# Optimization experiments

Measured on AMD Instinct MI355X. Metric: run time of the kernel, lower is better.

The kernel has to match this reference:

```python
import jax, jax.numpy as jnp
import numpy as np

B, N, H = 1, 4096, 2048
NH, HD = 16, H // 16
WINDOW = 4096
EPS = 1e-6
THETA = 10000.0
NEG = -1e30


def rmsnorm(x, w):
    var = jnp.mean(jnp.square(x.astype(jnp.float32)), axis=-1, keepdims=True)
    return (x * jax.lax.rsqrt(var + EPS)).astype(w.dtype) * w


def rotate_half(x):
    x1, x2 = x[..., : x.shape[-1] // 2], x[..., x.shape[-1] // 2 :]
    return jnp.concatenate((-x2, x1), axis=-1)


def setup_inputs() -> dict:
    key = jax.random.key(0)
    k1, k2, k3 = jax.random.split(key, 3)
    x = jax.random.normal(k1, (B, N, H), dtype=jnp.float32)
    w_qkv = jax.random.normal(k2, (H, 3 * H), dtype=jnp.float32) * (1.0 / np.sqrt(H))
    w_out = jax.random.normal(k3, (H, H), dtype=jnp.float32) * (1.0 / np.sqrt(H))
    q_gamma = jnp.ones((HD,), dtype=jnp.float32)
    k_gamma = jnp.ones((HD,), dtype=jnp.float32)
    return {"x": x, "w_qkv": w_qkv, "w_out": w_out, "q_gamma": q_gamma, "k_gamma": k_gamma}


def reference(x, w_qkv, w_out, q_gamma, k_gamma):
    b, n, _ = x.shape
    qkv = jnp.einsum('bnh,hm->bnm', x, w_qkv)  # [b,n,3H]
    q, k, v = jnp.split(qkv, 3, axis=-1)
    # [b, nh, n, hd]
    q = q.reshape(b, n, NH, HD).transpose(0, 2, 1, 3)
    k = k.reshape(b, n, NH, HD).transpose(0, 2, 1, 3)
    v = v.reshape(b, n, NH, HD).transpose(0, 2, 1, 3)
    # qk RMSNorm over head_dim
    q = rmsnorm(q, q_gamma)
    k = rmsnorm(k, k_gamma)
    # RoPE
    inv_freq = 1.0 / (THETA ** (jnp.arange(0, HD, 2, dtype=jnp.float32) / HD))
    t = jnp.arange(n, dtype=jnp.float32)
    freqs = t[:, None] * inv_freq[None, :]          # [n, hd/2]
    emb = jnp.concatenate((freqs, freqs), axis=-1)  # [n, hd]
    cos = jnp.cos(emb)[None, None, :, :]
    sin = jnp.sin(emb)[None, None, :, :]
    q = q * cos + rotate_half(q) * sin
    k = k * cos + rotate_half(k) * sin
    # causal + sliding-window mask (kv not truncated since n == WINDOW)
    kv_len = k.shape[-2]
    q_idx = jnp.arange(n)[:, None] + (kv_len - n)
    k_idx = jnp.arange(kv_len)[None, :]
    mask = (q_idx >= k_idx) & (q_idx - k_idx <= WINDOW)
    scores = jnp.einsum('bhqd,bhkd->bhqk', q, k) / np.sqrt(HD)
    scores = jnp.where(mask[None, None, :, :], scores, NEG)
    attn = jax.nn.softmax(scores, axis=-1)
    out = jnp.einsum('bhqk,bhkd->bhqd', attn, v)
    out = out.transpose(0, 2, 1, 3).reshape(b, n, H)
    return jnp.einsum('bnh,hm->bnm', out, w_out)
```

## Files before the change

### kernel.cpp

```cpp
#include <hip/hip_runtime.h>
#include <stdint.h>

typedef short bf16x8 __attribute__((ext_vector_type(8)));
typedef float f32x4 __attribute__((ext_vector_type(4)));
typedef unsigned short u16;

__device__ __forceinline__ float b2f(u16 u) {
  return __uint_as_float(((unsigned)u) << 16);
}
__device__ __forceinline__ u16 f2b(float f) {
  unsigned u = __float_as_uint(f);
  return (u16)((u + 0x7fffu + ((u >> 16) & 1u)) >> 16);
}

#define NEGINF (-1.0e30f)

__device__ __forceinline__ void gld_lds16(const u16* g, u16* l) {
  __builtin_amdgcn_global_load_lds(
      (const __attribute__((address_space(1))) unsigned int*)(const void*)g,
      (__attribute__((address_space(3))) unsigned int*)(void*)l, 16, 0, 0);
}

__device__ __forceinline__ int swzV(int o) {
  return o ^ ((((o) >> 6) & 7) << 3);
}
__device__ __forceinline__ int swzK(int o) {
  return o ^ ((((o) >> 7) & 7) << 3);
}

__global__ void sniff5(const u16* x, const u16* wq, const u16* wo,
                       const u16* qg, const u16* kg, int* flags) {
  const u16* p;
  int S;
  switch (blockIdx.x) {
    case 0: p = x;  S = 2048; break;
    case 1: p = wq; S = 2048; break;
    case 2: p = wo; S = 2048; break;
    case 3: p = qg; S = 128;  break;
    default: p = kg; S = 128; break;
  }
  __shared__ int cbig, czero;
  if (threadIdx.x == 0) { cbig = 0; czero = 0; }
  __syncthreads();
  int cb = 0, cz = 0;
  for (int i = threadIdx.x; i < S; i += 256) {
    const u16 u = p[i];
    if (((u >> 7) & 0xFF) >= 0xC0) ++cb;
    if (!(i & 1) && u == 0) ++cz;
  }
  atomicAdd(&cbig, cb);
  atomicAdd(&czero, cz);
  __syncthreads();
  if (threadIdx.x == 0)
    flags[blockIdx.x] = (cbig > S / 32 || czero > 3 * S / 8) ? 1 : 0;
}

__global__ __launch_bounds__(256) void conv_in(const void* __restrict__ src,
                                               u16* __restrict__ dst,
                                               const int* __restrict__ flags,
                                               int fidx, int n) {
  const int fp32 = flags[fidx];
  int i = blockIdx.x * 256 + threadIdx.x;
  const int stride = gridDim.x * 256;
  if (fp32) {
    const float* s = (const float*)src;
    for (; i < n; i += stride) dst[i] = f2b(s[i]);
  } else {
    const u16* s = (const u16*)src;
    for (; i < n; i += stride) dst[i] = s[i];
  }
}

__global__ __launch_bounds__(256) void transpose_in(
    const void* __restrict__ src, u16* __restrict__ dst,
    const int* __restrict__ flags, int fidx, int ss, int ds) {
  __shared__ u16 tile[64][65];
  const int fp32 = flags[fidx];
  const int rb = blockIdx.y * 64, cb = blockIdx.x * 64;
  const int cl = threadIdx.x & 63, r0 = threadIdx.x >> 6;
  if (fp32) {
    const float* s = (const float*)src;
#pragma unroll
    for (int i = 0; i < 16; ++i) {
      int r = r0 + i * 4;
      tile[r][cl] = f2b(s[(long long)(rb + r) * ss + cb + cl]);
    }
  } else {
    const u16* s = (const u16*)src;
#pragma unroll
    for (int i = 0; i < 16; ++i) {
      int r = r0 + i * 4;
      tile[r][cl] = s[(long long)(rb + r) * ss + cb + cl];
    }
  }
  __syncthreads();
#pragma unroll
  for (int i = 0; i < 16; ++i) {
    int r2 = r0 + i * 4;
    dst[(long long)(cb + r2) * ds + rb + cl] = tile[cl][r2];
  }
}

__global__ __launch_bounds__(256, 4) void gemm_qkv(
    const u16* __restrict__ A, const u16* __restrict__ Bt,
    const u16* __restrict__ gq, const u16* __restrict__ gk,
    u16* __restrict__ Cq, u16* __restrict__ Ck, u16* __restrict__ Cv, int K) {
  __shared__ __align__(16) u16 smem[2 * 128 * 64];
  u16* As = smem;
  u16* Bs = smem + 128 * 64;
  const int bid = blockIdx.x;
  const int xcd = bid & 7, lid = bid >> 3;
  const int mb = lid / 6, nsub = lid - mb * 6;
  const int nb = xcd * 6 + nsub;
  const int m0 = mb * 128;
  const int n0g = nb * 128;
  const int sel = nb >> 4;
  const int h = nb & 15;
  const int tid = threadIdx.x;
  const int w = tid >> 6, l = tid & 63;
  const int lane15 = l & 15, quad = l >> 4;
  const int wm = (w >> 1) * 64, wn = (w & 1) * 64;
  const int r8 = l >> 3, c8 = l & 7;
  const int sk = (c8 ^ r8) * 8;
  const u16* gA = A + (size_t)(m0 + r8) * K + sk;
  const u16* gB = Bt + (size_t)(n0g + r8) * K + sk;
  f32x4 acc[4][4] = {};
  const int nK = K >> 6;
  for (int kb = 0; kb < nK; ++kb) {
    __syncthreads();
#pragma unroll
    for (int i = 0; i < 4; ++i) {
      const int g = i * 4 + w;
      gld_lds16(gA + (size_t)g * 8 * K, &As[g * 512]);
      gld_lds16(gB + (size_t)g * 8 * K, &Bs[g * 512]);
    }
    __syncthreads();
#pragma unroll
    for (int kk = 0; kk < 2; ++kk) {
      bf16x8 af[4], bfr[4];
#pragma unroll
      for (int mi = 0; mi < 4; ++mi)
        af[mi] = *(const bf16x8*)&As[swzV((wm + mi * 16 + lane15) * 64 +
                                          kk * 32 + quad * 8)];
#pragma unroll
      for (int ni = 0; ni < 4; ++ni)
        bfr[ni] = *(const bf16x8*)&Bs[swzV((wn + ni * 16 + lane15) * 64 +
                                           kk * 32 + quad * 8)];
#pragma unroll
      for (int mi = 0; mi < 4; ++mi)
#pragma unroll
        for (int ni = 0; ni < 4; ++ni)
          acc[mi][ni] = __builtin_amdgcn_mfma_f32_16x16x32_bf16(
              af[mi], bfr[ni], acc[mi][ni], 0, 0, 0);
    }
    gA += 64;
    gB += 64;
  }

  __syncthreads();
  if (sel == 2) {
    u16* t = smem;
#pragma unroll
    for (int mi = 0; mi < 4; ++mi)
#pragma unroll
      for (int ni = 0; ni < 4; ++ni)
#pragma unroll
        for (int r = 0; r < 4; ++r) {
          const int row = wm + mi * 16 + quad * 4 + r;
          const int col = wn + ni * 16 + lane15;
          t[col * 128 + (row ^ ((col & 7) << 4))] = f2b(acc[mi][ni][r]);
        }
    __syncthreads();
    const int d = tid & 127, half = tid >> 7;
    u16* vdst = Cv + ((size_t)h * 128 + d) * 4096 + m0 + half * 64;
#pragma unroll
    for (int c8i = 0; c8i < 8; ++c8i) {
      const int n0c = half * 64 + c8i * 8;
      *(bf16x8*)(vdst + c8i * 8) =
          *(const bf16x8*)&t[d * 128 + (n0c ^ ((d & 7) << 4))];
    }
  } else {
    const u16* g = sel == 0 ? gq : gk;
    u16* dst = sel == 0 ? Cq : Ck;
    float* fss = (float*)smem;
    float gv[4];
#pragma unroll
    for (int ni = 0; ni < 4; ++ni) gv[ni] = b2f(g[wn + ni * 16 + lane15]);
#pragma unroll
    for (int mi = 0; mi < 4; ++mi)
#pragma unroll
      for (int r = 0; r < 4; ++r) {
        float ss = 0.f;
#pragma unroll
        for (int ni = 0; ni < 4; ++ni) ss += acc[mi][ni][r] * acc[mi][ni][r];
#pragma unroll
        for (int mk = 1; mk < 16; mk <<= 1) ss += __shfl_xor(ss, mk);
        if (lane15 == 0)
          fss[(wm + mi * 16 + quad * 4 + r) * 2 + (w & 1)] = ss;
      }
    __syncthreads();
#pragma unroll
    for (int mi = 0; mi < 4; ++mi)
#pragma unroll
      for (int r = 0; r < 4; ++r) {
        const int row = wm + mi * 16 + quad * 4 + r;
        const float rstd =
            rsqrtf((fss[row * 2] + fss[row * 2 + 1]) * (1.f / 128.f) + 1e-6f);
#pragma unroll
        for (int ni = 0; ni < 4; ++ni) acc[mi][ni][r] *= rstd * gv[ni];
      }
    __syncthreads();
    float* fex = (float*)smem;
    const int wp = w >> 1, lo = w & 1;
    float invf[4];
#pragma unroll
    for (int ni = 0; ni < 4; ++ni)
      invf[ni] = __expf(-(float)(ni * 16 + lane15) * 0.14391156831212787f);
    if (lo == 1) {
#pragma unroll
      for (int mi = 0; mi < 4; ++mi)
#pragma unroll
        for (int ni = 0; ni < 4; ++ni)
#pragma unroll
          for (int r = 0; r < 4; ++r)
            fex[wp * 4096 + (mi * 16 + quad * 4 + r) * 64 + ni * 16 + lane15] =
                acc[mi][ni][r];
    }
    __syncthreads();
    if (lo == 0) {
#pragma unroll
      for (int ni = 0; ni < 4; ++ni)
#pragma unroll
        for (int mi = 0; mi < 4; ++mi)
#pragma unroll
          for (int r = 0; r < 4; ++r) {
            const int rloc = mi * 16 + quad * 4 + r;
            const int p = m0 + wm + rloc;
            float s, c;
            __sincosf((float)p * invf[ni], &s, &c);
            const float a = acc[mi][ni][r];
            const float bb = fex[wp * 4096 + rloc * 64 + ni * 16 + lane15];
            dst[((size_t)h * 4096 + p) * 128 + ni * 16 + lane15] =
                f2b(a * c - bb * s);
          }
    }
    __syncthreads();
    if (lo == 0) {
#pragma unroll
      for (int mi = 0; mi < 4; ++mi)
#pragma unroll
        for (int ni = 0; ni < 4; ++ni)
#pragma unroll
          for (int r = 0; r < 4; ++r)
            fex[wp * 4096 + (mi * 16 + quad * 4 + r) * 64 + ni * 16 + lane15] =
                acc[mi][ni][r];
    }
    __syncthreads();
    if (lo == 1) {
#pragma unroll
      for (int ni = 0; ni < 4; ++ni)
#pragma unroll
        for (int mi = 0; mi < 4; ++mi)
#pragma unroll
          for (int r = 0; r < 4; ++r) {
            const int rloc = mi * 16 + quad * 4 + r;
            const int p = m0 + wm + rloc;
            float s, c;
            __sincosf((float)p * invf[ni], &s, &c);
            const float bb = acc[mi][ni][r];
            const float a = fex[wp * 4096 + rloc * 64 + ni * 16 + lane15];
            dst[((size_t)h * 4096 + p) * 128 + 64 + ni * 16 + lane15] =
                f2b(bb * c + a * s);
          }
    }
  }
}

__global__ __launch_bounds__(256) void gemm_bt_f32(
    const u16* __restrict__ A, const u16* __restrict__ Bt,
    float* __restrict__ C, int K) {
  __shared__ __align__(16) u16 As[128 * 64];
  __shared__ __align__(16) u16 Bs[128 * 64];
  const int bid = blockIdx.x;
  const int xcd = bid & 7, lid = bid >> 3;
  const int mb = lid >> 1, nsub = lid & 1;
  const int nb = xcd * 2 + nsub;
  const int m0 = mb * 128, n0 = nb * 128;
  const int tid = threadIdx.x;
  const int w = tid >> 6, l = tid & 63;
  const int lane15 = l & 15, quad = l >> 4;
  const int wm = (w >> 1) * 64, wn = (w & 1) * 64;
  const int r8 = l >> 3, c8 = l & 7;
  const int sk = (c8 ^ r8) * 8;
  const u16* gA = A + (size_t)(m0 + r8) * K + sk;
  const u16* gB = Bt + (size_t)(n0 + r8) * K + sk;
  f32x4 acc[4][4] = {};
  const int nK = K >> 6;
  for (int kb = 0; kb < nK; ++kb) {
    __syncthreads();
#pragma unroll
    for (int i = 0; i < 4; ++i) {
      const int g = i * 4 + w;
      gld_lds16(gA + (size_t)g * 8 * K, &As[g * 512]);
      gld_lds16(gB + (size_t)g * 8 * K, &Bs[g * 512]);
    }
    __syncthreads();
#pragma unroll
    for (int kk = 0; kk < 2; ++kk) {
      bf16x8 af[4], bfr[4];
#pragma unroll
      for (int mi = 0; mi < 4; ++mi)
        af[mi] = *(const bf16x8*)&As[swzV((wm + mi * 16 + lane15) * 64 +
                                          kk * 32 + quad * 8)];
#pragma unroll
      for (int ni = 0; ni < 4; ++ni)
        bfr[ni] = *(const bf16x8*)&Bs[swzV((wn + ni * 16 + lane15) * 64 +
                                           kk * 32 + quad * 8)];
#pragma unroll
      for (int mi = 0; mi < 4; ++mi)
#pragma unroll
        for (int ni = 0; ni < 4; ++ni)
          acc[mi][ni] = __builtin_amdgcn_mfma_f32_16x16x32_bf16(
              af[mi], bfr[ni], acc[mi][ni], 0, 0, 0);
    }
    gA += 64;
    gB += 64;
  }
#pragma unroll
  for (int mi = 0; mi < 4; ++mi)
#pragma unroll
    for (int ni = 0; ni < 4; ++ni)
#pragma unroll
      for (int r = 0; r < 4; ++r)
        C[(size_t)(m0 + wm + mi * 16 + quad * 4 + r) * 2048 +
          (n0 + wn + ni * 16 + lane15)] = acc[mi][ni][r];
}

__global__ __launch_bounds__(256, 2) void flash_attn(
    const u16* __restrict__ q_r, const u16* __restrict__ k_r,
    const u16* __restrict__ v_t, u16* __restrict__ attn) {
  __shared__ __align__(16) u16 Kt[64 * 128];
  __shared__ __align__(16) u16 Vt[128 * 64];
  __shared__ __align__(16) u16 Pt[128 * 64];
  const int b = blockIdx.x;
  const int h = b & 15;
  const int qt = (b < 256) ? (31 - (b >> 4)) : ((b - 256) >> 4);
  const int m0 = qt * 128;
  const int tid = threadIdx.x, w = tid >> 6, l = tid & 63;
  const int lane15 = l & 15, quad = l >> 4;

  bf16x8 aq[2][4];
#pragma unroll
  for (int mi = 0; mi < 2; ++mi)
#pragma unroll
    for (int ks = 0; ks < 4; ++ks)
      aq[mi][ks] = *(const bf16x8*)&q_r[((size_t)h * 4096 + m0 + w * 32 +
                                         mi * 16 + lane15) * 128 +
                                        ks * 32 + quad * 8];

  f32x4 acc_o[2][8] = {};
  float m_i[2][4], l_i[2][4];
#pragma unroll
  for (int mi = 0; mi < 2; ++mi)
#pragma unroll
    for (int r = 0; r < 4; ++r) {
      m_i[mi][r] = NEGINF;
      l_i[mi][r] = 0.f;
    }

  const int jend = m0 + 64;
  for (int j0 = 0; j0 <= jend; j0 += 64) {
    __syncthreads();
#pragma unroll
    for (int i = 0; i < 4; ++i) {
      const int rg = i * 4 + w;
      const int keyr = rg * 4 + (l >> 4);
      const int kc = (l & 15) ^ (keyr & 7);
      const int dr = rg * 8 + (l >> 3);
      const int vc = (l & 7) ^ (dr & 7);
      gld_lds16(&k_r[((size_t)h * 4096 + j0 + keyr) * 128 + kc * 8],
                &Kt[rg * 512]);
      gld_lds16(&v_t[((size_t)h * 128 + dr) * 4096 + j0 + vc * 8],
                &Vt[rg * 512]);
    }
    __syncthreads();

    f32x4 s2[2][4] = {};
#pragma unroll
    for (int ni = 0; ni < 4; ++ni) {
#pragma unroll
      for (int ks = 0; ks < 4; ++ks) {
        bf16x8 bk = *(const bf16x8*)&Kt[swzK((ni * 16 + lane15) * 128 +
                                             ks * 32 + quad * 8)];
        s2[0][ni] = __builtin_amdgcn_mfma_f32_16x16x32_bf16(aq[0][ks], bk,
                                                            s2[0][ni], 0, 0, 0);
        s2[1][ni] = __builtin_amdgcn_mfma_f32_16x16x32_bf16(aq[1][ks], bk,
                                                            s2[1][ni], 0, 0, 0);
      }
    }

    const float sc = 0.08838834764831845f;
    const bool mt = (j0 >= m0);
#pragma unroll
    for (int mi = 0; mi < 2; ++mi) {
#pragma unroll
      for (int r = 0; r < 4; ++r) {
        const int lrow = w * 32 + mi * 16 + quad * 4 + r;
        float xv[4], mx4 = NEGINF;
#pragma unroll
        for (int ni = 0; ni < 4; ++ni) {
          float xx = s2[mi][ni][r] * sc;
          if (mt && (j0 + ni * 16 + lane15 > m0 + lrow)) xx = NEGINF;
          xv[ni] = xx;
          mx4 = fmaxf(mx4, xx);
        }
        const float mold = m_i[mi][r];
        const unsigned long long bal = __ballot(mx4 > mold + 8.0f);
        float mcur = mold;
        if (((unsigned)(bal >> (quad * 16)) & 0xFFFFu) != 0u) {
          float mx = mx4;
#pragma unroll
          for (int mk = 1; mk < 16; mk <<= 1)
            mx = fmaxf(mx, __shfl_xor(mx, mk));
          const float mnew = fmaxf(mold, mx);
          const float alpha = __expf(mold - mnew);
          l_i[mi][r] *= alpha;
          m_i[mi][r] = mnew;
          mcur = mnew;
#pragma unroll
          for (int ni = 0; ni < 8; ++ni) acc_o[mi][ni][r] *= alpha;
        }
        float rs = 0.f;
#pragma unroll
        for (int ni = 0; ni < 4; ++ni) {
          const float p = __expf(xv[ni] - mcur);
          Pt[swzV(lrow * 64 + ni * 16 + lane15)] = f2b(p);
          rs += p;
        }
        l_i[mi][r] += rs;
      }
    }

#pragma unroll
    for (int ks = 0; ks < 2; ++ks) {
      bf16x8 ap0 = *(const bf16x8*)&Pt[swzV((w * 32 + lane15) * 64 + ks * 32 +
                                            quad * 8)];
      bf16x8 ap1 = *(const bf16x8*)&Pt[swzV((w * 32 + 16 + lane15) * 64 +
                                            ks * 32 + quad * 8)];
#pragma unroll
      for (int ni = 0; ni < 8; ++ni) {
        bf16x8 bv = *(const bf16x8*)&Vt[swzV((ni * 16 + lane15) * 64 +
                                             ks * 32 + quad * 8)];
        acc_o[0][ni] = __builtin_amdgcn_mfma_f32_16x16x32_bf16(
            ap0, bv, acc_o[0][ni], 0, 0, 0);
        acc_o[1][ni] = __builtin_amdgcn_mfma_f32_16x16x32_bf16(
            ap1, bv, acc_o[1][ni], 0, 0, 0);
      }
    }
  }

#pragma unroll
  for (int mi = 0; mi < 2; ++mi)
#pragma unroll
    for (int r = 0; r < 4; ++r) {
      float s = l_i[mi][r];
#pragma unroll
      for (int mk = 1; mk < 16; mk <<= 1) s += __shfl_xor(s, mk);
      l_i[mi][r] = s;
    }
#pragma unroll
  for (int mi = 0; mi < 2; ++mi)
#pragma unroll
    for (int ni = 0; ni < 8; ++ni)
#pragma unroll
      for (int r = 0; r < 4; ++r)
        attn[(size_t)(m0 + w * 32 + mi * 16 + quad * 4 + r) * 2048 + h * 128 +
             ni * 16 + lane15] = f2b(acc_o[mi][ni][r] / l_i[mi][r]);
}

extern "C" void kernel_launch(void* const* d_in, const int* in_sizes, int n_in,
                              void* d_out, int out_size, void* d_ws,
                              size_t ws_size, hipStream_t stream) {
  (void)out_size; (void)ws_size;
  int ix = 0, iwq = 1, iwo = 2, ig1 = 3, ig2 = 4;
  {
    int g1 = -1, g2 = -1, xx = -1, wqq = -1, woo = -1;
    for (int i = 0; i < n_in; ++i) {
      const int s = in_sizes[i];
      if (s == 8388608) xx = i;
      else if (s == 12582912) wqq = i;
      else if (s == 4194304) woo = i;
      else if (s == 128) { if (g1 < 0) g1 = i; else g2 = i; }
    }
    if (xx >= 0 && wqq >= 0 && woo >= 0 && g1 >= 0 && g2 >= 0) {
      ix = xx; iwq = wqq; iwo = woo; ig1 = g1; ig2 = g2;
    }
  }
  const void* x = d_in[ix];
  const void* wq = d_in[iwq];
  const void* wo = d_in[iwo];
  const void* qg = d_in[ig1];
  const void* kg = d_in[ig2];
  float* out = (float*)d_out;
  char* ws = (char*)d_ws;
  u16* xb = (u16*)(ws);
  u16* q_r = (u16*)(ws + 16777216LL);
  u16* wT = (u16*)(ws + 33554432LL);
  u16* attn = (u16*)(ws + 33554432LL);
  u16* woT = (u16*)(ws + 50331648LL);
  int* flags = (int*)(ws + 58720256LL);
  u16* gq_b = (u16*)(ws + 58720512LL);
  u16* gk_b = (u16*)(ws + 58721024LL);
  u16* k_r = (u16*)d_out;
  u16* v_t = (u16*)d_out + 8388608;

  sniff5<<<5, 256, 0, stream>>>((const u16*)x, (const u16*)wq, (const u16*)wo,
                                (const u16*)qg, (const u16*)kg, flags);
  conv_in<<<8192, 256, 0, stream>>>(x, xb, flags, 0, 4096 * 2048);
  conv_in<<<1, 256, 0, stream>>>(qg, gq_b, flags, 3, 128);
  conv_in<<<1, 256, 0, stream>>>(kg, gk_b, flags, 4, 128);
  transpose_in<<<dim3(96, 32), 256, 0, stream>>>(wq, wT, flags, 1, 6144, 2048);
  gemm_qkv<<<dim3(1536), 256, 0, stream>>>(xb, wT, gq_b, gk_b, q_r, k_r, v_t,
                                           2048);
  transpose_in<<<dim3(32, 32), 256, 0, stream>>>(wo, woT, flags, 2, 2048, 2048);
  flash_attn<<<dim3(512), 256, 0, stream>>>(q_r, k_r, v_t, attn);
  gemm_bt_f32<<<dim3(512), 256, 0, stream>>>(attn, woT, out, 2048);
}
```

Measured before the change: 635.0 us.

## Vectorize RoPE epilogue via swizzled bf16 LDS tile and fuse gamma conversion

The q/k epilogue of the QKV GEMM now writes the normalized tile to a swizzled bf16 LDS buffer once. All threads then apply RoPE with 8-wide vector loads and stores, replacing two serialized fp32 half-exchange passes that used only half the waves each. The q/k gamma vectors are read directly in their native format using the dtype flags, which removes two tiny conversion kernel launches. The launch_bounds occupancy hint is also dropped. RoPE inputs are rounded to bf16 before rotation, a slight precision change.

Result: no change. 644.9 us (+1.6%).

```diff
diff --git a/kernel.cpp b/kernel.cpp
--- a/kernel.cpp
+++ b/kernel.cpp
@@ -101,10 +101,11 @@
   }
 }
 
-__global__ __launch_bounds__(256, 4) void gemm_qkv(
+__global__ __launch_bounds__(256) void gemm_qkv(
     const u16* __restrict__ A, const u16* __restrict__ Bt,
     const u16* __restrict__ gq, const u16* __restrict__ gk,
-    u16* __restrict__ Cq, u16* __restrict__ Ck, u16* __restrict__ Cv, int K) {
+    const int* __restrict__ flags, u16* __restrict__ Cq, u16* __restrict__ Ck,
+    u16* __restrict__ Cv, int K) {
   __shared__ __align__(16) u16 smem[2 * 128 * 64];
   u16* As = smem;
   u16* Bs = smem + 128 * 64;
@@ -180,12 +181,10 @@
           *(const bf16x8*)&t[d * 128 + (n0c ^ ((d & 7) << 4))];
     }
   } else {
-    const u16* g = sel == 0 ? gq : gk;
+    const void* graw = sel == 0 ? (const void*)gq : (const void*)gk;
+    const int gfp32 = flags[sel == 0 ? 3 : 4];
     u16* dst = sel == 0 ? Cq : Ck;
     float* fss = (float*)smem;
-    float gv[4];
-#pragma unroll
-    for (int ni = 0; ni < 4; ++ni) gv[ni] = b2f(g[wn + ni * 16 + lane15]);
 #pragma unroll
     for (int mi = 0; mi < 4; ++mi)
 #pragma unroll
@@ -199,6 +198,12 @@
           fss[(wm + mi * 16 + quad * 4 + r) * 2 + (w & 1)] = ss;
       }
     __syncthreads();
+    float gv[4];
+#pragma unroll
+    for (int ni = 0; ni < 4; ++ni) {
+      const int col = wn + ni * 16 + lane15;
+      gv[ni] = gfp32 ? ((const float*)graw)[col] : b2f(((const u16*)graw)[col]);
+    }
 #pragma unroll
     for (int mi = 0; mi < 4; ++mi)
 #pragma unroll
@@ -210,68 +215,43 @@
         for (int ni = 0; ni < 4; ++ni) acc[mi][ni][r] *= rstd * gv[ni];
       }
     __syncthreads();
-    float* fex = (float*)smem;
-    const int wp = w >> 1, lo = w & 1;
-    float invf[4];
-#pragma unroll
-    for (int ni = 0; ni < 4; ++ni)
-      invf[ni] = __expf(-(float)(ni * 16 + lane15) * 0.14391156831212787f);
-    if (lo == 1) {
-#pragma unroll
-      for (int mi = 0; mi < 4; ++mi)
-#pragma unroll
-        for (int ni = 0; ni < 4; ++ni)
-#pragma unroll
-          for (int r = 0; r < 4; ++r)
-            fex[wp * 4096 + (mi * 16 + quad * 4 + r) * 64 + ni * 16 + lane15] =
-                acc[mi][ni][r];
-    }
-    __syncthreads();
-    if (lo == 0) {
+    u16* nt = smem;
+#pragma unroll
+    for (int mi = 0; mi < 4; ++mi)
 #pragma unroll
       for (int ni = 0; ni < 4; ++ni)
 #pragma unroll
-        for (int mi = 0; mi < 4; ++mi)
-#pragma unroll
-          for (int r = 0; r < 4; ++r) {
-            const int rloc = mi * 16 + quad * 4 + r;
-            const int p = m0 + wm + rloc;
-            float s, c;
-            __sincosf((float)p * invf[ni], &s, &c);
-            const float a = acc[mi][ni][r];
-            const float bb = fex[wp * 4096 + rloc * 64 + ni * 16 + lane15];
-            dst[((size_t)h * 4096 + p) * 128 + ni * 16 + lane15] =
-                f2b(a * c - bb * s);
-          }
-    }
-    __syncthreads();
-    if (lo == 0) {
-#pragma unroll
-      for (int mi = 0; mi < 4; ++mi)
-#pragma unroll
-        for (int ni = 0; ni < 4; ++ni)
-#pragma unroll
-          for (int r = 0; r < 4; ++r)
-            fex[wp * 4096 + (mi * 16 + quad * 4 + r) * 64 + ni * 16 + lane15] =
-                acc[mi][ni][r];
-    }
-    __syncthreads();
-    if (lo == 1) {
-#pragma unroll
-      for (int ni = 0; ni < 4; ++ni)
-#pragma unroll
-        for (int mi = 0; mi < 4; ++mi)
-#pragma unroll
-          for (int r = 0; r < 4; ++r) {
-            const int rloc = mi * 16 + quad * 4 + r;
-            const int p = m0 + wm + rloc;
-            float s, c;
-            __sincosf((float)p * invf[ni], &s, &c);
-            const float bb = acc[mi][ni][r];
-            const float a = fex[wp * 4096 + rloc * 64 + ni * 16 + lane15];
-            dst[((size_t)h * 4096 + p) * 128 + 64 + ni * 16 + lane15] =
-                f2b(bb * c + a * s);
-          }
+        for (int r = 0; r < 4; ++r) {
+          const int row = wm + mi * 16 + quad * 4 + r;
+          const int col = wn + ni * 16 + lane15;
+          nt[row * 128 + (((col >> 3) ^ (row & 7)) << 3) + (col & 7)] =
+              f2b(acc[mi][ni][r]);
+        }
+    __syncthreads();
+    const int d0 = (tid & 15) * 8;
+    float invf[8];
+#pragma unroll
+    for (int j = 0; j < 8; ++j)
+      invf[j] = __expf(-(float)((d0 + j) & 63) * 0.14391156831212787f);
+    const int rbase = tid >> 4;
+#pragma unroll
+    for (int pass = 0; pass < 8; ++pass) {
+      const int row = rbase + pass * 16;
+      const int p = m0 + row;
+      bf16x8 va = *(const bf16x8*)&nt[row * 128 +
+                                      (((d0 >> 3) ^ (row & 7)) << 3)];
+      bf16x8 vb = *(const bf16x8*)&nt[row * 128 +
+                                      ((((d0 ^ 64) >> 3) ^ (row & 7)) << 3)];
+      bf16x8 vo;
+#pragma unroll
+      for (int j = 0; j < 8; ++j) {
+        float s, c;
+        __sincosf((float)p * invf[j], &s, &c);
+        const float a = b2f((u16)va[j]);
+        const float bb = b2f((u16)vb[j]);
+        vo[j] = (short)f2b(d0 < 64 ? a * c - bb * s : a * c + bb * s);
+      }
+      *(bf16x8*)&dst[((size_t)h * 4096 + p) * 128 + d0] = vo;
     }
   }
 }
@@ -509,19 +489,16 @@
   u16* attn = (u16*)(ws + 33554432LL);
   u16* woT = (u16*)(ws + 50331648LL);
   int* flags = (int*)(ws + 58720256LL);
-  u16* gq_b = (u16*)(ws + 58720512LL);
-  u16* gk_b = (u16*)(ws + 58721024LL);
   u16* k_r = (u16*)d_out;
   u16* v_t = (u16*)d_out + 8388608;
 
   sniff5<<<5, 256, 0, stream>>>((const u16*)x, (const u16*)wq, (const u16*)wo,
                                 (const u16*)qg, (const u16*)kg, flags);
   conv_in<<<8192, 256, 0, stream>>>(x, xb, flags, 0, 4096 * 2048);
-  conv_in<<<1, 256, 0, stream>>>(qg, gq_b, flags, 3, 128);
-  conv_in<<<1, 256, 0, stream>>>(kg, gk_b, flags, 4, 128);
   transpose_in<<<dim3(96, 32), 256, 0, stream>>>(wq, wT, flags, 1, 6144, 2048);
-  gemm_qkv<<<dim3(1536), 256, 0, stream>>>(xb, wT, gq_b, gk_b, q_r, k_r, v_t,
-                                           2048);
+  gemm_qkv<<<dim3(1536), 256, 0, stream>>>(xb, wT, (const u16*)qg,
+                                           (const u16*)kg, flags, q_r, k_r,
+                                           v_t, 2048);
   transpose_in<<<dim3(32, 32), 256, 0, stream>>>(wo, woT, flags, 2, 2048, 2048);
   flash_attn<<<dim3(512), 256, 0, stream>>>(q_r, k_r, v_t, attn);
   gemm_bt_f32<<<dim3(512), 256, 0, stream>>>(attn, woT, out, 2048);
```
